# Kernel tuning notes

Measured on AMD Instinct MI355X. Metric: run time of the kernel, lower is better.

The kernel has to match this reference:

```python
import jax, jax.numpy as jnp
import numpy as np

N = 50000          # n_nodes
E_RAND = 800000    # random edges (before self-loops)
D_FEAT = 128
ALPHA = 0.1
NITER = 10


def setup_inputs() -> dict:
    key = jax.random.key(0)
    k1, k2, k3 = jax.random.split(key, 3)
    r = jax.random.randint(k1, (E_RAND,), 0, N)
    c = jax.random.randint(k2, (E_RAND,), 0, N)
    loop = jnp.arange(N)
    # A + I  (self-loops appended, matching calc_A_hat's sp.eye addition)
    rows = jnp.concatenate([r, loop]).astype(jnp.int32)   # [850000]
    cols = jnp.concatenate([c, loop]).astype(jnp.int32)   # [850000]
    # D_vec = row sums of (A + I); symmetric normalization D^-1/2 (A+I) D^-1/2
    deg = jax.ops.segment_sum(jnp.ones(rows.shape[0], jnp.float32), rows, num_segments=N)
    dinv = 1.0 / jnp.sqrt(jnp.maximum(deg, 1.0))
    # A_hat values pre-scaled by (1 - alpha), as registered in the buffer
    vals = ((1.0 - ALPHA) * dinv[rows] * dinv[cols]).astype(jnp.float32)
    E = jax.random.normal(k3, (N, D_FEAT), dtype=jnp.float32)
    return {"E": E, "rows": rows, "cols": cols, "vals": vals}


def reference(E, rows, cols, vals):
    # preds_{t+1} = A_hat @ preds_t + alpha * E   (niter power-iteration steps)
    # spmm via gather + segment_sum over the COO edge list.
    def step(preds, _):
        msg = vals[:, None] * preds[cols]                       # [nnz, d]
        preds = jax.ops.segment_sum(msg, rows, num_segments=N) + ALPHA * E
        return preds, None
    out, _ = jax.lax.scan(step, E, None, length=NITER)
    return out
```

## Files before the change

kernel.cpp:

```cpp
#include <hip/hip_runtime.h>


#define ALPHA 0.1f
#define NITER 10
#define DFEAT 128
#define CHUNK 1024


__global__ void hist_rows(const int* __restrict__ rows, int* __restrict__ counts, int nnz) {
    int e = blockIdx.x * blockDim.x + threadIdx.x;
    if (e < nnz) atomicAdd(&counts[rows[e]], 1);
}

__global__ void scan_reduce(const int* __restrict__ counts, int* __restrict__ blockSums, int N) {
    __shared__ int lds[256];
    int b = blockIdx.x, t = threadIdx.x;
    int base = b * CHUNK + t * 4;
    int s = 0;
    if (base + 4 <= N) {
        int4 v = *(const int4*)(counts + base);
        s = v.x + v.y + v.z + v.w;
    } else {
        for (int k = 0; k < 4; ++k) if (base + k < N) s += counts[base + k];
    }
    lds[t] = s;
    __syncthreads();
    for (int off = 128; off > 0; off >>= 1) {
        if (t < off) lds[t] += lds[t + off];
        __syncthreads();
    }
    if (t == 0) blockSums[b] = lds[0];
}

__global__ void scan_blocksums(const int* __restrict__ blockSums, int* __restrict__ blockOff,
                               int* __restrict__ rowptr, int NB, int N) {
    __shared__ int lds[1024];
    int t = threadIdx.x;
    int v = (t < NB) ? blockSums[t] : 0;
    lds[t] = v;
    __syncthreads();
    for (int off = 1; off < 1024; off <<= 1) {
        int u = (t >= off) ? lds[t - off] : 0;
        __syncthreads();
        lds[t] += u;
        __syncthreads();
    }
    if (t < NB) blockOff[t] = (t == 0) ? 0 : lds[t - 1];
    if (t == 1023) rowptr[N] = lds[1023];
}

__global__ void scan_write(const int* __restrict__ counts, const int* __restrict__ blockOff,
                           int* __restrict__ rowptr, int* __restrict__ offs, int N) {
    __shared__ int lds[256];
    int b = blockIdx.x, t = threadIdx.x;
    int base = b * CHUNK + t * 4;
    int c0 = 0, c1 = 0, c2 = 0, c3 = 0;
    if (base + 4 <= N) {
        int4 v = *(const int4*)(counts + base);
        c0 = v.x; c1 = v.y; c2 = v.z; c3 = v.w;
    } else {
        if (base + 0 < N) c0 = counts[base + 0];
        if (base + 1 < N) c1 = counts[base + 1];
        if (base + 2 < N) c2 = counts[base + 2];
        if (base + 3 < N) c3 = counts[base + 3];
    }
    int s = c0 + c1 + c2 + c3;
    lds[t] = s;
    __syncthreads();
    for (int off = 1; off < 256; off <<= 1) {
        int u = (t >= off) ? lds[t - off] : 0;
        __syncthreads();
        lds[t] += u;
        __syncthreads();
    }
    int run = ((t == 0) ? 0 : lds[t - 1]) + blockOff[b];
    if (base + 0 < N) { rowptr[base + 0] = run; offs[base + 0] = run; run += c0; }
    if (base + 1 < N) { rowptr[base + 1] = run; offs[base + 1] = run; run += c1; }
    if (base + 2 < N) { rowptr[base + 2] = run; offs[base + 2] = run; run += c2; }
    if (base + 3 < N) { rowptr[base + 3] = run; offs[base + 3] = run; run += c3; }
}

__global__ void build_csr(const int* __restrict__ rows, const int* __restrict__ cols,
                          const float* __restrict__ vals, int* __restrict__ offsets,
                          int2* __restrict__ packed, int nnz) {
    int e = blockIdx.x * blockDim.x + threadIdx.x;
    if (e >= nnz) return;
    int r = rows[e];
    int pos = atomicAdd(&offsets[r], 1);
    int2 p;
    p.x = cols[e] << 8;
    p.y = __float_as_int(vals[e]);
    packed[pos] = p;
}


__device__ inline unsigned f32_to_bf16_rne(float f) {
    unsigned x = __float_as_uint(f);
    return (x + 0x7fffu + ((x >> 16) & 1u)) >> 16;
}

__global__ void cvt_f32_bf16(const float2* __restrict__ in, unsigned* __restrict__ out, int n2) {
    int i = blockIdx.x * blockDim.x + threadIdx.x;
    if (i < n2) {
        float2 v = in[i];
        out[i] = f32_to_bf16_rne(v.x) | (f32_to_bf16_rne(v.y) << 16);
    }
}


#define GATH(k)                                                                   \
    int2 p##k = packed[i + k];                                                    \
    uint4 x##k = *(const uint4*)(srcb + (size_t)(unsigned)p##k.x + soff);

#define ACC(k)                                                                    \
    {   float v = __int_as_float(p##k.y);                                         \
        acc[0] += v * __uint_as_float(x##k.x << 16);                              \
        acc[1] += v * __uint_as_float(x##k.x & 0xffff0000u);                      \
        acc[2] += v * __uint_as_float(x##k.y << 16);                              \
        acc[3] += v * __uint_as_float(x##k.y & 0xffff0000u);                      \
        acc[4] += v * __uint_as_float(x##k.z << 16);                              \
        acc[5] += v * __uint_as_float(x##k.z & 0xffff0000u);                      \
        acc[6] += v * __uint_as_float(x##k.w << 16);                              \
        acc[7] += v * __uint_as_float(x##k.w & 0xffff0000u); }

template <bool DSTB>
__global__ void spmm_quad(const int* __restrict__ rowptr, const int2* __restrict__ packed,
                          const char* __restrict__ srcb, const float* __restrict__ E,
                          void* __restrict__ dst, int N) {
    int wave = (blockIdx.x * blockDim.x + threadIdx.x) >> 6;
    int nwav = (gridDim.x * blockDim.x) >> 6;
    int lane = threadIdx.x & 63;
    int g    = lane >> 4;
    int sub  = lane & 15;
    const size_t soff = (size_t)sub * 16;

    for (int w4 = wave * 4; w4 < N; w4 += nwav * 4) {
        int w = w4 + g;
        if (w >= N) w = N - 1;
        bool valid = (w4 + g < N);

        int s = rowptr[w];
        int e = rowptr[w + 1];

        float acc[8];
        {
            const float4* ep = (const float4*)(E + (size_t)w * DFEAT + sub * 8);
            float4 e0 = ep[0], e1 = ep[1];
            acc[0] = ALPHA * e0.x; acc[1] = ALPHA * e0.y;
            acc[2] = ALPHA * e0.z; acc[3] = ALPHA * e0.w;
            acc[4] = ALPHA * e1.x; acc[5] = ALPHA * e1.y;
            acc[6] = ALPHA * e1.z; acc[7] = ALPHA * e1.w;
        }

        int i = s;
        for (; i + 4 <= e; i += 4) {
            GATH(0) GATH(1) GATH(2) GATH(3)
            ACC(0) ACC(1) ACC(2) ACC(3)
        }
        for (; i < e; ++i) {
            GATH(0)
            ACC(0)
        }

        if (valid) {
            if constexpr (DSTB) {
                uint4 o;
                o.x = f32_to_bf16_rne(acc[0]) | (f32_to_bf16_rne(acc[1]) << 16);
                o.y = f32_to_bf16_rne(acc[2]) | (f32_to_bf16_rne(acc[3]) << 16);
                o.z = f32_to_bf16_rne(acc[4]) | (f32_to_bf16_rne(acc[5]) << 16);
                o.w = f32_to_bf16_rne(acc[6]) | (f32_to_bf16_rne(acc[7]) << 16);
                *(uint4*)((char*)dst + (size_t)w * 256 + soff) = o;
            } else {
                float4* op = (float4*)((float*)dst + (size_t)w * DFEAT + sub * 8);
                op[0] = make_float4(acc[0], acc[1], acc[2], acc[3]);
                op[1] = make_float4(acc[4], acc[5], acc[6], acc[7]);
            }
        }
    }
}

#undef GATH
#undef ACC

extern "C" void kernel_launch(void* const* d_in, const int* in_sizes, int n_in,
                              void* d_out, int out_size, void* d_ws, size_t ws_size,
                              hipStream_t stream) {
    const float* E    = (const float*)d_in[0];
    const int*   rows = (const int*)d_in[1];
    const int*   cols = (const int*)d_in[2];
    const float* vals = (const float*)d_in[3];
    float*       out  = (float*)d_out;

    const int nd  = in_sizes[0];
    const int nnz = in_sizes[1];
    const int N   = nd / DFEAT;
    const int NB  = (N + CHUNK - 1) / CHUNK;

    const int Np  = (N + 4 + 3) & ~3;
    const int NBp = (NB + 3) & ~3;
    char* ws = (char*)d_ws;
    char*  bufA    = ws;
    char*  bufB    = ws + (size_t)nd * 2;
    int*   rowptr  = (int*)(ws + (size_t)nd * 4);
    int*   offs    = rowptr + Np;
    int*   bsums   = offs + Np;
    int*   boff    = bsums + NBp;
    int2*  packed  = (int2*)((char*)(boff + NBp));

    dim3 blk(256);
    dim3 gE((nnz + 255) / 256);

    hipMemsetAsync(offs, 0, (size_t)N * 4, stream);
    hist_rows<<<gE, blk, 0, stream>>>(rows, offs, nnz);
    scan_reduce<<<NB, 256, 0, stream>>>(offs, bsums, N);
    scan_blocksums<<<1, 1024, 0, stream>>>(bsums, boff, rowptr, NB, N);
    scan_write<<<NB, 256, 0, stream>>>(offs, boff, rowptr, offs, N);
    build_csr<<<gE, blk, 0, stream>>>(rows, cols, vals, offs, packed, nnz);

    const int n2 = nd / 2;
    cvt_f32_bf16<<<(n2 + 255) / 256, blk, 0, stream>>>((const float2*)E, (unsigned*)bufB, n2);

    dim3 gS(2048);
    char* cur = bufB;
    char* nxt = bufA;
    for (int it = 1; it <= NITER - 1; ++it) {
        spmm_quad<true><<<gS, blk, 0, stream>>>(rowptr, packed, cur, E, nxt, N);
        char* t = cur; cur = nxt; nxt = t;
    }
    spmm_quad<false><<<gS, blk, 0, stream>>>(rowptr, packed, cur, E, out, N);
}
```

Measured before the change: 445.8 us.

## Read bf16 E in SpMM iterations, vectorize edge loads, size grid to rows

Intermediate iterations now read the alpha*E term from a bf16 copy of E, held in the output buffer, instead of the fp32 E. This halves that stream's bytes. The packed edge array is realigned to 16 bytes and read as int4 pairs after a peel step for odd start indices, cutting load instruction count. The persistent 2048-block grid is replaced by a grid sized to about two quads per wave. The bf16 E slightly changes numerics in the intermediate iterations.

```diff
diff --git a/kernel.cpp b/kernel.cpp
--- a/kernel.cpp
+++ b/kernel.cpp
@@ -108,25 +108,24 @@
 }
 
 
-#define GATH(k)                                                                   \
-    int2 p##k = packed[i + k];                                                    \
-    uint4 x##k = *(const uint4*)(srcb + (size_t)(unsigned)p##k.x + soff);
-
-#define ACC(k)                                                                    \
-    {   float v = __int_as_float(p##k.y);                                         \
-        acc[0] += v * __uint_as_float(x##k.x << 16);                              \
-        acc[1] += v * __uint_as_float(x##k.x & 0xffff0000u);                      \
-        acc[2] += v * __uint_as_float(x##k.y << 16);                              \
-        acc[3] += v * __uint_as_float(x##k.y & 0xffff0000u);                      \
-        acc[4] += v * __uint_as_float(x##k.z << 16);                              \
-        acc[5] += v * __uint_as_float(x##k.z & 0xffff0000u);                      \
-        acc[6] += v * __uint_as_float(x##k.w << 16);                              \
-        acc[7] += v * __uint_as_float(x##k.w & 0xffff0000u); }
+#define XPND(u)  __uint_as_float((u) << 16), __uint_as_float((u) & 0xffff0000u)
+
+#define GACC(cofs, vbits)                                                         \
+    {   uint4 x = *(const uint4*)(srcb + (size_t)(unsigned)(cofs) + soff);        \
+        float v = __int_as_float(vbits);                                          \
+        acc[0] += v * __uint_as_float(x.x << 16);                                 \
+        acc[1] += v * __uint_as_float(x.x & 0xffff0000u);                         \
+        acc[2] += v * __uint_as_float(x.y << 16);                                 \
+        acc[3] += v * __uint_as_float(x.y & 0xffff0000u);                         \
+        acc[4] += v * __uint_as_float(x.z << 16);                                 \
+        acc[5] += v * __uint_as_float(x.z & 0xffff0000u);                         \
+        acc[6] += v * __uint_as_float(x.w << 16);                                 \
+        acc[7] += v * __uint_as_float(x.w & 0xffff0000u); }
 
 template <bool DSTB>
 __global__ void spmm_quad(const int* __restrict__ rowptr, const int2* __restrict__ packed,
-                          const char* __restrict__ srcb, const float* __restrict__ E,
-                          void* __restrict__ dst, int N) {
+                          const char* __restrict__ srcb, const char* __restrict__ Eb,
+                          const float* __restrict__ Ef, void* __restrict__ dst, int N) {
     int wave = (blockIdx.x * blockDim.x + threadIdx.x) >> 6;
     int nwav = (gridDim.x * blockDim.x) >> 6;
     int lane = threadIdx.x & 63;
@@ -143,8 +142,18 @@
         int e = rowptr[w + 1];
 
         float acc[8];
-        {
-            const float4* ep = (const float4*)(E + (size_t)w * DFEAT + sub * 8);
+        if constexpr (DSTB) {
+            uint4 ev = *(const uint4*)(Eb + (size_t)w * 256 + soff);
+            acc[0] = ALPHA * __uint_as_float(ev.x << 16);
+            acc[1] = ALPHA * __uint_as_float(ev.x & 0xffff0000u);
+            acc[2] = ALPHA * __uint_as_float(ev.y << 16);
+            acc[3] = ALPHA * __uint_as_float(ev.y & 0xffff0000u);
+            acc[4] = ALPHA * __uint_as_float(ev.z << 16);
+            acc[5] = ALPHA * __uint_as_float(ev.z & 0xffff0000u);
+            acc[6] = ALPHA * __uint_as_float(ev.w << 16);
+            acc[7] = ALPHA * __uint_as_float(ev.w & 0xffff0000u);
+        } else {
+            const float4* ep = (const float4*)(Ef + (size_t)w * DFEAT + sub * 8);
             float4 e0 = ep[0], e1 = ep[1];
             acc[0] = ALPHA * e0.x; acc[1] = ALPHA * e0.y;
             acc[2] = ALPHA * e0.z; acc[3] = ALPHA * e0.w;
@@ -153,13 +162,22 @@
         }
 
         int i = s;
+        if (i < e && (i & 1)) {
+            int2 p = packed[i];
+            GACC(p.x, p.y)
+            ++i;
+        }
         for (; i + 4 <= e; i += 4) {
-            GATH(0) GATH(1) GATH(2) GATH(3)
-            ACC(0) ACC(1) ACC(2) ACC(3)
+            int4 q0 = *(const int4*)(packed + i);
+            int4 q1 = *(const int4*)(packed + i + 2);
+            GACC(q0.x, q0.y)
+            GACC(q0.z, q0.w)
+            GACC(q1.x, q1.y)
+            GACC(q1.z, q1.w)
         }
         for (; i < e; ++i) {
-            GATH(0)
-            ACC(0)
+            int2 p = packed[i];
+            GACC(p.x, p.y)
         }
 
         if (valid) {
@@ -179,8 +197,8 @@
     }
 }
 
-#undef GATH
-#undef ACC
+#undef GACC
+#undef XPND
 
 extern "C" void kernel_launch(void* const* d_in, const int* in_sizes, int n_in,
                               void* d_out, int out_size, void* d_ws, size_t ws_size,
@@ -205,7 +223,10 @@
     int*   offs    = rowptr + Np;
     int*   bsums   = offs + Np;
     int*   boff    = bsums + NBp;
-    int2*  packed  = (int2*)((char*)(boff + NBp));
+    size_t pk_off  = (((size_t)nd * 4 + (size_t)(2 * Np + 2 * NBp) * 4) + 15) & ~(size_t)15;
+    int2*  packed  = (int2*)(ws + pk_off);
+
+    char* Eb = (char*)d_out;
 
     dim3 blk(256);
     dim3 gE((nnz + 255) / 256);
@@ -218,14 +239,19 @@
     build_csr<<<gE, blk, 0, stream>>>(rows, cols, vals, offs, packed, nnz);
 
     const int n2 = nd / 2;
-    cvt_f32_bf16<<<(n2 + 255) / 256, blk, 0, stream>>>((const float2*)E, (unsigned*)bufB, n2);
-
-    dim3 gS(2048);
-    char* cur = bufB;
+    cvt_f32_bf16<<<(n2 + 255) / 256, blk, 0, stream>>>((const float2*)E, (unsigned*)Eb, n2);
+
+    int quads  = (N + 3) / 4;
+    int waves  = (quads + 1) / 2;
+    int blocks = (waves + 3) / 4;
+    dim3 gS(blocks);
+
+    char* cur = Eb;
     char* nxt = bufA;
     for (int it = 1; it <= NITER - 1; ++it) {
-        spmm_quad<true><<<gS, blk, 0, stream>>>(rowptr, packed, cur, E, nxt, N);
-        char* t = cur; cur = nxt; nxt = t;
-    }
-    spmm_quad<false><<<gS, blk, 0, stream>>>(rowptr, packed, cur, E, out, N);
-}
+        spmm_quad<true><<<gS, blk, 0, stream>>>(rowptr, packed, cur, Eb, E, nxt, N);
+        cur = nxt;
+        nxt = (cur == bufA) ? bufB : bufA;
+    }
+    spmm_quad<false><<<gS, blk, 0, stream>>>(rowptr, packed, cur, Eb, E, out, N);
+}
```

New measurement: 440.7 us. Within noise of the previous version (-1.1%).
